# Kernel optimization log

Hardware: AMD Instinct MI355X
Metric: run time of the kernel (lower is better)

The kernel has to match this reference:

```python
import jax, jax.numpy as jnp
import numpy as np

B, C_IN, N, F_OUT = 16, 128, 2048, 64
NEG_SLOPE = 0.33
MASK_VAL = -9e15


def setup_inputs() -> dict:
    key = jax.random.key(0)
    k1, k2, k3, k4 = jax.random.split(key, 4)
    h = jax.random.normal(k1, (B, C_IN, N, 1), dtype=jnp.float32)
    g = jax.random.normal(k2, (B, 1, N, N), dtype=jnp.float32)
    # xavier_uniform with gain=1.414
    gain = 1.414
    lim_W = gain * np.sqrt(6.0 / (C_IN + F_OUT))
    W = jax.random.uniform(k3, (C_IN, F_OUT), minval=-lim_W, maxval=lim_W, dtype=jnp.float32)
    lim_a = gain * np.sqrt(6.0 / (2 * F_OUT + 1))
    a = jax.random.uniform(k4, (2 * F_OUT, 1), minval=-lim_a, maxval=lim_a, dtype=jnp.float32)
    return {"h": h, "g": g, "W": W, "a": a}


def reference(h, g, W, a):
    # h: [B, C, N, 1] -> node features [B, N, C]
    hn = jnp.transpose(h[..., 0], (0, 2, 1))
    Wh = jnp.einsum('bnc,cf->bnf', hn, W)  # [B, N, F]
    F = W.shape[1]
    a1, a2 = a[:F, 0], a[F:, 0]
    # additive attention: e[i,j] = leakyrelu(Wh[i]@a1 + Wh[j]@a2)
    e = jax.nn.leaky_relu((Wh @ a1)[:, :, None] + (Wh @ a2)[:, None, :], NEG_SLOPE)  # [B,N,N]
    mask = g[:, 0] > 0  # [B, N, N]
    attn = jax.nn.softmax(jnp.where(mask, e, MASK_VAL), axis=-1)
    h_prime = jnp.einsum('bij,bjf->bif', attn, Wh)  # [B, N, F]
    return jnp.transpose(h_prime, (0, 2, 1))[..., None]  # [B, F, N, 1]
```

## Files before the change

### kernel.cpp

```cpp
#include <hip/hip_runtime.h>
#include <hip/hip_bf16.h>

#define NB 16
#define NC 128
#define NN 2048
#define NF 64
#define NEG_SLOPE 0.33f
#define MASK_VAL (-9.0e15f)

typedef float    f32x4 __attribute__((ext_vector_type(4)));
typedef _Float16 f16x4 __attribute__((ext_vector_type(4)));
typedef _Float16 f16x8 __attribute__((ext_vector_type(8)));

__device__ __forceinline__ float lrelu(float x) {
    return x > 0.0f ? x : x * NEG_SLOPE;
}

__global__ __launch_bounds__(256) void k_precompute(
    const float* __restrict__ h, const float* __restrict__ W,
    const float* __restrict__ a, _Float16* __restrict__ wht,
    float* __restrict__ s1g, float* __restrict__ s2g)
{
    __shared__ float Wl[64 * 64];
    __shared__ float ht[64 * 129];

    const int t = threadIdx.x;
    const int b = blockIdx.x >> 5;
    const int n0 = (blockIdx.x & 31) << 6;
    const int lane = t & 63, cg = t >> 6;

    #pragma unroll 8
    for (int k = 0; k < 32; ++k) {
        const int c = cg * 32 + k;
        ht[lane * 129 + c] = h[(size_t)(b * NC + c) * NN + n0 + lane];
    }

    const int fg = t & 15, ns = t >> 4;
    f32x4 acc[4] = {};
    for (int half = 0; half < 2; ++half) {
        if (half) __syncthreads();
        #pragma unroll
        for (int k = 0; k < 4; ++k) {
            const int idx = k * 1024 + t * 4;
            *(f32x4*)&Wl[idx] = *(const f32x4*)&W[half * 4096 + idx];
        }
        __syncthreads();
        #pragma unroll 4
        for (int c2 = 0; c2 < 64; ++c2) {
            const f32x4 wv = *(const f32x4*)&Wl[c2 * 64 + fg * 4];
            #pragma unroll
            for (int m = 0; m < 4; ++m) {
                const float hv = ht[(ns * 4 + m) * 129 + half * 64 + c2];
                acc[m] += wv * hv;
            }
        }
    }

    const f32x4 a1v = *(const f32x4*)&a[fg * 4];
    const f32x4 a2v = *(const f32x4*)&a[NF + fg * 4];
    #pragma unroll
    for (int m = 0; m < 4; ++m) {
        float p1 = acc[m].x * a1v.x + acc[m].y * a1v.y + acc[m].z * a1v.z + acc[m].w * a1v.w;
        float p2 = acc[m].x * a2v.x + acc[m].y * a2v.y + acc[m].z * a2v.z + acc[m].w * a2v.w;
        #pragma unroll
        for (int d = 1; d < 16; d <<= 1) {
            p1 += __shfl_xor(p1, d, 64);
            p2 += __shfl_xor(p2, d, 64);
        }
        if (fg == 0) {
            const int n = n0 + ns * 4 + m;
            s1g[(size_t)b * NN + n] = p1;
            s2g[(size_t)b * NN + n] = p2;
        }
    }
    #pragma unroll
    for (int q = 0; q < 4; ++q) {
        f16x4 v;
        v[0] = (_Float16)acc[0][q]; v[1] = (_Float16)acc[1][q];
        v[2] = (_Float16)acc[2][q]; v[3] = (_Float16)acc[3][q];
        const int f = fg * 4 + q;
        *(f16x4*)&wht[((size_t)b * NF + f) * NN + n0 + ns * 4] = v;
    }
}

__global__ __launch_bounds__(512, 8) void k_attn(
    const float* __restrict__ g, const _Float16* __restrict__ wht,
    const float* __restrict__ s1g, const float* __restrict__ s2g,
    float* __restrict__ out)
{
    __shared__ float s2b[NN];
    __shared__ float s1b[16];
    __shared__ float Srow[16];
    __shared__ float alphaL[2 * 16];
    __shared__ _Float16 Pc[2 * 16 * 264];
    __shared__ float scratch[1024];

    const int t = threadIdx.x;
    const int lane = t & 63;
    const int w = t >> 6;
    const int b = blockIdx.x >> 7;
    const int i0 = (blockIdx.x & 127) << 4;

    *(f32x4*)&s2b[t * 4] = *(const f32x4*)&s2g[(size_t)b * NN + t * 4];
    if (t < 16) s1b[t] = s1g[(size_t)b * NN + i0 + t];
    __syncthreads();

    const float* gb = g + (size_t)b * NN * NN;
    const float* gr0 = gb + (size_t)(i0 + w) * NN + lane * 4;
    const float* gr1 = gr0 + 8 * NN;
    const float s1r0 = s1b[w];
    const float s1r1 = s1b[w + 8];

    const int nt = w & 3, kh = w >> 2;
    const int arow = lane & 15;
    const int koff = (lane >> 4) * 8;
    const _Float16* wb = wht + ((size_t)b * NF + nt * 16 + arow) * NN;

    float m0 = MASK_VAL, m1 = MASK_VAL;
    float su0 = 0.0f, su1 = 0.0f;
    f32x4 acc = {0.0f, 0.0f, 0.0f, 0.0f};

    f32x4 c0 = *(const f32x4*)gr0;
    f32x4 c1 = *(const f32x4*)gr1;

    for (int ch = 0; ch < 8; ++ch) {
        f32x4 n0 = c0, n1 = c1;
        if (ch < 7) {
            n0 = *(const f32x4*)(gr0 + (ch + 1) * 256);
            n1 = *(const f32x4*)(gr1 + (ch + 1) * 256);
        }
        const int pb = (ch & 1) * 16 * 264;
        const f32x4 sv = *(const f32x4*)&s2b[ch * 256 + lane * 4];

        {
            float e0 = c0.x > 0.0f ? lrelu(s1r0 + sv.x) : MASK_VAL;
            float e1 = c0.y > 0.0f ? lrelu(s1r0 + sv.y) : MASK_VAL;
            float e2 = c0.z > 0.0f ? lrelu(s1r0 + sv.z) : MASK_VAL;
            float e3 = c0.w > 0.0f ? lrelu(s1r0 + sv.w) : MASK_VAL;
            float cm = fmaxf(fmaxf(e0, e1), fmaxf(e2, e3));
            #pragma unroll
            for (int d = 1; d < 64; d <<= 1) cm = fmaxf(cm, __shfl_xor(cm, d, 64));
            const float mn = fmaxf(m0, cm);
            const float al = __expf(m0 - mn);
            m0 = mn;
            const float p0 = __expf(e0 - mn), p1 = __expf(e1 - mn);
            const float p2 = __expf(e2 - mn), p3 = __expf(e3 - mn);
            su0 = su0 * al + ((p0 + p1) + (p2 + p3));
            f16x4 pv; pv[0] = (_Float16)p0; pv[1] = (_Float16)p1;
            pv[2] = (_Float16)p2; pv[3] = (_Float16)p3;
            *(f16x4*)&Pc[pb + w * 264 + lane * 4] = pv;
            if (lane == 0) alphaL[(ch & 1) * 16 + w] = al;
        }
        {
            float e0 = c1.x > 0.0f ? lrelu(s1r1 + sv.x) : MASK_VAL;
            float e1 = c1.y > 0.0f ? lrelu(s1r1 + sv.y) : MASK_VAL;
            float e2 = c1.z > 0.0f ? lrelu(s1r1 + sv.z) : MASK_VAL;
            float e3 = c1.w > 0.0f ? lrelu(s1r1 + sv.w) : MASK_VAL;
            float cm = fmaxf(fmaxf(e0, e1), fmaxf(e2, e3));
            #pragma unroll
            for (int d = 1; d < 64; d <<= 1) cm = fmaxf(cm, __shfl_xor(cm, d, 64));
            const float mn = fmaxf(m1, cm);
            const float al = __expf(m1 - mn);
            m1 = mn;
            const float p0 = __expf(e0 - mn), p1 = __expf(e1 - mn);
            const float p2 = __expf(e2 - mn), p3 = __expf(e3 - mn);
            su1 = su1 * al + ((p0 + p1) + (p2 + p3));
            f16x4 pv; pv[0] = (_Float16)p0; pv[1] = (_Float16)p1;
            pv[2] = (_Float16)p2; pv[3] = (_Float16)p3;
            *(f16x4*)&Pc[pb + (w + 8) * 264 + lane * 4] = pv;
            if (lane == 0) alphaL[(ch & 1) * 16 + w + 8] = al;
        }

        __syncthreads();

        {
            const f32x4 av = *(const f32x4*)&alphaL[(ch & 1) * 16 + (lane >> 4) * 4];
            acc.x *= av.x; acc.y *= av.y; acc.z *= av.z; acc.w *= av.w;
            const _Float16* wbc = wb + ch * 256;
            #pragma unroll
            for (int ks = 0; ks < 4; ++ks) {
                const int kc = kh * 128 + ks * 32;
                f16x8 af = *(const f16x8*)&Pc[pb + arow * 264 + kc + koff];
                f16x8 bf = *(const f16x8*)&wbc[kc + koff];
                acc = __builtin_amdgcn_mfma_f32_16x16x32_f16(af, bf, acc, 0, 0, 0);
            }
        }
        c0 = n0; c1 = n1;
    }

    {
        float s = su0;
        #pragma unroll
        for (int d = 1; d < 64; d <<= 1) s += __shfl_xor(s, d, 64);
        if (lane == 0) Srow[w] = s;
        s = su1;
        #pragma unroll
        for (int d = 1; d < 64; d <<= 1) s += __shfl_xor(s, d, 64);
        if (lane == 0) Srow[w + 8] = s;
    }
    if (kh == 1) *(f32x4*)&scratch[(nt * 64 + lane) * 4] = acc;
    __syncthreads();
    if (kh == 0) {
        f32x4 o = *(const f32x4*)&scratch[(nt * 64 + lane) * 4];
        acc.x += o.x; acc.y += o.y; acc.z += o.z; acc.w += o.w;
        const int rbase = (lane >> 4) * 4;
        f32x4 res;
        #pragma unroll
        for (int r2 = 0; r2 < 4; ++r2) res[r2] = acc[r2] * (1.0f / Srow[rbase + r2]);
        const int f = nt * 16 + arow;
        *(f32x4*)&out[((size_t)b * NF + f) * NN + (size_t)(i0 + rbase)] = res;
    }
}

extern "C" void kernel_launch(void* const* d_in, const int* in_sizes, int n_in,
                              void* d_out, int out_size, void* d_ws, size_t ws_size,
                              hipStream_t stream)
{
    (void)in_sizes; (void)n_in; (void)out_size; (void)ws_size;
    const float* h = (const float*)d_in[0];
    const float* g = (const float*)d_in[1];
    const float* W = (const float*)d_in[2];
    const float* a = (const float*)d_in[3];
    float* out = (float*)d_out;

    char* ws = (char*)d_ws;
    _Float16* wht = (_Float16*)ws;
    float* s1 = (float*)(ws + (size_t)NB * NF * NN * sizeof(_Float16));
    float* s2 = s1 + (size_t)NB * NN;

    k_precompute<<<NB * (NN / 64), 256, 0, stream>>>(h, W, a, wht, s1, s2);
    k_attn<<<NB * (NN / 16), 512, 0, stream>>>(g, wht, s1, s2, out);
}
```

Before: 105.2 us.

## Use a static per-row softmax max bound and deepen the mask prefetch

Because leaky ReLU is monotone, each row's maximum logit is bounded by lrelu(s1_i + max_j s2_j). The kernel now computes that bound once per block with a block-wide max over s2, replacing the online softmax. This drops the per-chunk wave-wide max shuffles, the alpha rescale exps, the alpha shared-memory traffic and the accumulator rescaling. The g-mask loads are also double-buffered two chunks ahead and the chunk loop is fully unrolled, to keep more memory requests in flight. The risks are that a fully masked row now yields a zero sum instead of a uniform distribution, and that fp16 probabilities could underflow if the unmasked maximum sits well below the bound.

```diff
diff --git a/kernel.cpp b/kernel.cpp
--- a/kernel.cpp
+++ b/kernel.cpp
@@ -91,7 +91,7 @@
     __shared__ float s2b[NN];
     __shared__ float s1b[16];
     __shared__ float Srow[16];
-    __shared__ float alphaL[2 * 16];
+    __shared__ float wred[8];
     __shared__ _Float16 Pc[2 * 16 * 264];
     __shared__ float scratch[1024];
 
@@ -101,81 +101,75 @@
     const int b = blockIdx.x >> 7;
     const int i0 = (blockIdx.x & 127) << 4;
 
-    *(f32x4*)&s2b[t * 4] = *(const f32x4*)&s2g[(size_t)b * NN + t * 4];
+    const f32x4 s2v = *(const f32x4*)&s2g[(size_t)b * NN + t * 4];
+    *(f32x4*)&s2b[t * 4] = s2v;
     if (t < 16) s1b[t] = s1g[(size_t)b * NN + i0 + t];
+    float lm = fmaxf(fmaxf(s2v.x, s2v.y), fmaxf(s2v.z, s2v.w));
+    #pragma unroll
+    for (int d = 1; d < 64; d <<= 1) lm = fmaxf(lm, __shfl_xor(lm, d, 64));
+    if (lane == 0) wred[w] = lm;
     __syncthreads();
+    float S2MAX = wred[0];
+    #pragma unroll
+    for (int q = 1; q < 8; ++q) S2MAX = fmaxf(S2MAX, wred[q]);
 
     const float* gb = g + (size_t)b * NN * NN;
     const float* gr0 = gb + (size_t)(i0 + w) * NN + lane * 4;
     const float* gr1 = gr0 + 8 * NN;
     const float s1r0 = s1b[w];
     const float s1r1 = s1b[w + 8];
+    const float Mr0 = lrelu(s1r0 + S2MAX);
+    const float Mr1 = lrelu(s1r1 + S2MAX);
 
     const int nt = w & 3, kh = w >> 2;
     const int arow = lane & 15;
     const int koff = (lane >> 4) * 8;
     const _Float16* wb = wht + ((size_t)b * NF + nt * 16 + arow) * NN;
 
-    float m0 = MASK_VAL, m1 = MASK_VAL;
     float su0 = 0.0f, su1 = 0.0f;
     f32x4 acc = {0.0f, 0.0f, 0.0f, 0.0f};
 
-    f32x4 c0 = *(const f32x4*)gr0;
-    f32x4 c1 = *(const f32x4*)gr1;
-
+    f32x4 r0[2], r1[2];
+    r0[0] = *(const f32x4*)gr0;
+    r1[0] = *(const f32x4*)gr1;
+    r0[1] = *(const f32x4*)(gr0 + 256);
+    r1[1] = *(const f32x4*)(gr1 + 256);
+
+    #pragma unroll
     for (int ch = 0; ch < 8; ++ch) {
-        f32x4 n0 = c0, n1 = c1;
-        if (ch < 7) {
-            n0 = *(const f32x4*)(gr0 + (ch + 1) * 256);
-            n1 = *(const f32x4*)(gr1 + (ch + 1) * 256);
-        }
-        const int pb = (ch & 1) * 16 * 264;
+        const int sl = ch & 1;
+        const f32x4 c0 = r0[sl], c1 = r1[sl];
+        if (ch < 6) {
+            r0[sl] = *(const f32x4*)(gr0 + (ch + 2) * 256);
+            r1[sl] = *(const f32x4*)(gr1 + (ch + 2) * 256);
+        }
+        const int pb = sl * 16 * 264;
         const f32x4 sv = *(const f32x4*)&s2b[ch * 256 + lane * 4];
 
         {
-            float e0 = c0.x > 0.0f ? lrelu(s1r0 + sv.x) : MASK_VAL;
-            float e1 = c0.y > 0.0f ? lrelu(s1r0 + sv.y) : MASK_VAL;
-            float e2 = c0.z > 0.0f ? lrelu(s1r0 + sv.z) : MASK_VAL;
-            float e3 = c0.w > 0.0f ? lrelu(s1r0 + sv.w) : MASK_VAL;
-            float cm = fmaxf(fmaxf(e0, e1), fmaxf(e2, e3));
-            #pragma unroll
-            for (int d = 1; d < 64; d <<= 1) cm = fmaxf(cm, __shfl_xor(cm, d, 64));
-            const float mn = fmaxf(m0, cm);
-            const float al = __expf(m0 - mn);
-            m0 = mn;
-            const float p0 = __expf(e0 - mn), p1 = __expf(e1 - mn);
-            const float p2 = __expf(e2 - mn), p3 = __expf(e3 - mn);
-            su0 = su0 * al + ((p0 + p1) + (p2 + p3));
+            const float p0 = c0.x > 0.0f ? __expf(lrelu(s1r0 + sv.x) - Mr0) : 0.0f;
+            const float p1 = c0.y > 0.0f ? __expf(lrelu(s1r0 + sv.y) - Mr0) : 0.0f;
+            const float p2 = c0.z > 0.0f ? __expf(lrelu(s1r0 + sv.z) - Mr0) : 0.0f;
+            const float p3 = c0.w > 0.0f ? __expf(lrelu(s1r0 + sv.w) - Mr0) : 0.0f;
+            su0 += (p0 + p1) + (p2 + p3);
             f16x4 pv; pv[0] = (_Float16)p0; pv[1] = (_Float16)p1;
             pv[2] = (_Float16)p2; pv[3] = (_Float16)p3;
             *(f16x4*)&Pc[pb + w * 264 + lane * 4] = pv;
-            if (lane == 0) alphaL[(ch & 1) * 16 + w] = al;
         }
         {
-            float e0 = c1.x > 0.0f ? lrelu(s1r1 + sv.x) : MASK_VAL;
-            float e1 = c1.y > 0.0f ? lrelu(s1r1 + sv.y) : MASK_VAL;
-            float e2 = c1.z > 0.0f ? lrelu(s1r1 + sv.z) : MASK_VAL;
-            float e3 = c1.w > 0.0f ? lrelu(s1r1 + sv.w) : MASK_VAL;
-            float cm = fmaxf(fmaxf(e0, e1), fmaxf(e2, e3));
-            #pragma unroll
-            for (int d = 1; d < 64; d <<= 1) cm = fmaxf(cm, __shfl_xor(cm, d, 64));
-            const float mn = fmaxf(m1, cm);
-            const float al = __expf(m1 - mn);
-            m1 = mn;
-            const float p0 = __expf(e0 - mn), p1 = __expf(e1 - mn);
-            const float p2 = __expf(e2 - mn), p3 = __expf(e3 - mn);
-            su1 = su1 * al + ((p0 + p1) + (p2 + p3));
+            const float p0 = c1.x > 0.0f ? __expf(lrelu(s1r1 + sv.x) - Mr1) : 0.0f;
+            const float p1 = c1.y > 0.0f ? __expf(lrelu(s1r1 + sv.y) - Mr1) : 0.0f;
+            const float p2 = c1.z > 0.0f ? __expf(lrelu(s1r1 + sv.z) - Mr1) : 0.0f;
+            const float p3 = c1.w > 0.0f ? __expf(lrelu(s1r1 + sv.w) - Mr1) : 0.0f;
+            su1 += (p0 + p1) + (p2 + p3);
             f16x4 pv; pv[0] = (_Float16)p0; pv[1] = (_Float16)p1;
             pv[2] = (_Float16)p2; pv[3] = (_Float16)p3;
             *(f16x4*)&Pc[pb + (w + 8) * 264 + lane * 4] = pv;
-            if (lane == 0) alphaL[(ch & 1) * 16 + w + 8] = al;
         }
 
         __syncthreads();
 
         {
-            const f32x4 av = *(const f32x4*)&alphaL[(ch & 1) * 16 + (lane >> 4) * 4];
-            acc.x *= av.x; acc.y *= av.y; acc.z *= av.z; acc.w *= av.w;
             const _Float16* wbc = wb + ch * 256;
             #pragma unroll
             for (int ks = 0; ks < 4; ++ks) {
@@ -185,7 +179,6 @@
                 acc = __builtin_amdgcn_mfma_f32_16x16x32_f16(af, bf, acc, 0, 0, 0);
             }
         }
-        c0 = n0; c1 = n1;
     }
 
     {
```

Result: slower. 130.2 us (+23.8%).
